# Kernel tuning notes

Measured on AMD Instinct MI355X. Metric: run time of the kernel, lower is better.

## Reference

```python
import jax, jax.numpy as jnp
import numpy as np

B, N, NFEAT = 64, 384, 16
E = 3
NHID, NOUT = 128, 128
ST_HID, ST_OUT = 64, 16


def _xavier(key, shape, fan_in, fan_out):
    a = jnp.sqrt(6.0 / (fan_in + fan_out))
    return jax.random.uniform(key, shape, jnp.float32, -a, a)


def setup_inputs() -> dict:
    key = jax.random.key(0)
    ks = jax.random.split(key, 10)
    x = jax.random.normal(ks[0], (B, N, NFEAT), jnp.float32)
    adj = jax.random.uniform(ks[1], (B, E, N, N), jnp.float32)
    emb_w = _xavier(ks[2], (NFEAT, NFEAT), NFEAT, NFEAT)            # Linear(nfeat,nfeat,bias=False)
    gc1_w = _xavier(ks[3], (E, NFEAT, NHID), NFEAT, NHID)           # (edge_dim,in,out)
    gc2_w = _xavier(ks[4], (E, NHID, NHID), NHID, NHID)             # single middle layer (num_layers-2=1)
    gc3_w = _xavier(ks[5], (E, NHID, NOUT), NHID, NOUT)
    st_w1 = _xavier(ks[6], (ST_HID, NOUT), NOUT, ST_HID)            # nn.Linear stores (out,in)
    st_b1 = jnp.zeros((ST_HID,), jnp.float32)
    st_w2 = jnp.full((2 * ST_OUT, ST_HID), 1e-10, jnp.float32)      # init.constant_(linear2.weight, 1e-10)
    st_b2 = jnp.zeros((2 * ST_OUT,), jnp.float32)
    rescale_w = jnp.zeros((1,), jnp.float32)                        # Rescale weight init zero
    return {"x": x, "adj": adj, "emb_w": emb_w, "gc1_w": gc1_w, "gc2_w": gc2_w,
            "gc3_w": gc3_w, "st_w1": st_w1, "st_b1": st_b1, "st_w2": st_w2,
            "st_b2": st_b2, "rescale_w": rescale_w}


def _rgcn_layer(h, adj, W, relu):
    # support: einsum('bid,edh->beih'), aggregate: einsum('beij,bejh->beih'), then sum over e
    support = jnp.einsum('bnd,edh->benh', h, W)
    out = jnp.einsum('bemn,benh->bemh', adj, support)
    if relu:
        out = jax.nn.relu(out)
    return out.sum(axis=1)  # aggregate='sum' over edge types


def reference(x, adj, emb_w, gc1_w, gc2_w, gc3_w, st_w1, st_b1, st_w2, st_b2, rescale_w):
    h = x @ emb_w.T                                   # emb Linear, no bias
    h = _rgcn_layer(h, adj, gc1_w, True)
    h = _rgcn_layer(h, adj, gc2_w, True)
    h = _rgcn_layer(h, adj, gc3_w, False)             # gc3: use_relu=False
    flat = h.reshape(-1, h.shape[-1])                 # (B*N, nout)
    z = jnp.tanh(flat @ st_w1.T + st_b1) @ st_w2.T + st_b2
    s, t = z[:, :ST_OUT], z[:, ST_OUT:]
    s = jnp.exp(rescale_w) * jnp.tanh(s)              # Rescale(tanh(s))
    return jnp.stack([s, t])                          # (2, B*N, ST_OUT)
```

## Files before the change

### kernel.cpp

```cpp
#include <hip/hip_runtime.h>
#include <math.h>

#define ROWS 24576
#define ADJ_BE (384*384)

typedef _Float16 h4v __attribute__((ext_vector_type(4)));
typedef _Float16 h8v __attribute__((ext_vector_type(8)));
typedef float f32x4 __attribute__((ext_vector_type(4)));

#define SPLIT_SCALE 2048.0f
#define INV_SPLIT_SCALE (1.0f / 2048.0f)

__global__ __launch_bounds__(256) void k_h0split(const float* __restrict__ x,
        const float* __restrict__ emb_w, _Float16* __restrict__ Hh, _Float16* __restrict__ Hl) {
    __shared__ float embL[256];
    int t = threadIdx.x;
    if (t < 64) *(float4*)&embL[4 * t] = *(const float4*)(emb_w + 4 * t);
    __syncthreads();
    int gid = blockIdx.x * 256 + t;
    int b = gid / 384, r = gid % 384;
    const float* xp = x + (size_t)gid * 16;
    float xr[16];
    *(float4*)&xr[0]  = *(const float4*)(xp);
    *(float4*)&xr[4]  = *(const float4*)(xp + 4);
    *(float4*)&xr[8]  = *(const float4*)(xp + 8);
    *(float4*)&xr[12] = *(const float4*)(xp + 12);
    size_t base = (size_t)b * 16 * 384 + r;
#pragma unroll
    for (int d = 0; d < 16; ++d) {
        float acc = 0.f;
#pragma unroll
        for (int k = 0; k < 16; ++k) acc = fmaf(xr[k], embL[d * 16 + k], acc);
        _Float16 h = (_Float16)acc;
        Hh[base + (size_t)d * 384] = h;
        Hl[base + (size_t)d * 384] = (_Float16)((acc - (float)h) * SPLIT_SCALE);
    }
}

__global__ __launch_bounds__(256) void k_adj16(const float* __restrict__ adj,
        const _Float16* __restrict__ Hh, const _Float16* __restrict__ Hl,
        float* __restrict__ T1) {
    int mt = blockIdx.x, e = blockIdx.y, b = blockIdx.z;
    const float* A = adj + (size_t)(b * 3 + e) * ADJ_BE + (size_t)mt * 64 * 384;
    const _Float16* BH = Hh + (size_t)b * 16 * 384;
    const _Float16* BL = Hl + (size_t)b * 16 * 384;

    __shared__ _Float16 Af[2][4][4][17][8];

    int t = threadIdx.x;
    int wave = t >> 6, lane = t & 63;
    int l16 = lane & 15, quad = lane >> 4;
    int r0s = t >> 3, q4s = t & 7;

    f32x4 acc0 = f32x4{0.f, 0.f, 0.f, 0.f};
    f32x4 acc1 = f32x4{0.f, 0.f, 0.f, 0.f};

    float4 ra[2];
    h8v rbh, rbl;
#pragma unroll
    for (int p = 0; p < 2; ++p)
        ra[p] = *(const float4*)(A + (size_t)(r0s + 32 * p) * 384 + 4 * q4s);
    rbh = *(const h8v*)(BH + (size_t)l16 * 384 + 8 * quad);
    rbl = *(const h8v*)(BL + (size_t)l16 * 384 + 8 * quad);

    for (int kc = 0; kc < 12; ++kc) {
#pragma unroll
        for (int p = 0; p < 2; ++p) {
            int r = r0s + 32 * p;
            float vv[4] = {ra[p].x, ra[p].y, ra[p].z, ra[p].w};
            h4v hh, ll;
#pragma unroll
            for (int c = 0; c < 4; ++c) {
                _Float16 h = (_Float16)vv[c];
                hh[c] = h;
                ll[c] = (_Float16)((vv[c] - (float)h) * SPLIT_SCALE);
            }
            *(h4v*)&Af[0][r >> 4][q4s >> 1][r & 15][(q4s & 1) * 4] = hh;
            *(h4v*)&Af[1][r >> 4][q4s >> 1][r & 15][(q4s & 1) * 4] = ll;
        }
        h8v b_h = rbh, b_l = rbl;
        __syncthreads();
        if (kc + 1 < 12) {
            int kn = (kc + 1) * 32;
#pragma unroll
            for (int p = 0; p < 2; ++p)
                ra[p] = *(const float4*)(A + (size_t)(r0s + 32 * p) * 384 + kn + 4 * q4s);
            rbh = *(const h8v*)(BH + (size_t)l16 * 384 + kn + 8 * quad);
            rbl = *(const h8v*)(BL + (size_t)l16 * 384 + kn + 8 * quad);
        }
        h8v a_h = *(const h8v*)&Af[0][wave][quad][l16][0];
        h8v a_l = *(const h8v*)&Af[1][wave][quad][l16][0];
        acc0 = __builtin_amdgcn_mfma_f32_16x16x32_f16(a_h, b_h, acc0, 0, 0, 0);
        acc1 = __builtin_amdgcn_mfma_f32_16x16x32_f16(a_h, b_l, acc1, 0, 0, 0);
        acc1 = __builtin_amdgcn_mfma_f32_16x16x32_f16(a_l, b_h, acc1, 0, 0, 0);
        __syncthreads();
    }
    float* Tp = T1 + ((size_t)(b * 3 + e) * 384 + (size_t)mt * 64 + wave * 16) * 16;
#pragma unroll
    for (int reg = 0; reg < 4; ++reg) {
        float v = fmaf(acc1[reg], INV_SPLIT_SCALE, acc0[reg]);
        Tp[(quad * 4 + reg) * 16 + l16] = v;
    }
}

__global__ __launch_bounds__(256) void k_l1s2(const float* __restrict__ T1,
        const float* __restrict__ W1, float* __restrict__ h1) {
    __shared__ float wL[3][16][128];
    __shared__ float tL[3][64][17];
    int t = threadIdx.x;
    int rt = blockIdx.x;
    int b = rt / 6, m0 = (rt % 6) * 64;
#pragma unroll
    for (int p = 0; p < 6; ++p) {
        int idx = t + p * 256;
        float4 v = *(const float4*)(W1 + (size_t)idx * 4);
        int e = idx / 512, rem = idx % 512;
        int d = rem >> 5, q = rem & 31;
        *(float4*)&wL[e][d][q * 4] = v;
    }
#pragma unroll
    for (int p = 0; p < 3; ++p) {
        int idx = t + p * 256;
        int e = idx >> 8, rem = idx & 255;
        int r = rem >> 2, q = rem & 3;
        float4 v = *(const float4*)(T1 + ((size_t)(b * 3 + e) * 384 + m0 + r) * 16 + q * 4);
        tL[e][r][q*4+0] = v.x; tL[e][r][q*4+1] = v.y; tL[e][r][q*4+2] = v.z; tL[e][r][q*4+3] = v.w;
    }
    __syncthreads();
    int tx = t & 31;
    int ty = t >> 5;
    float tot[8][4] = {};
#pragma unroll
    for (int e = 0; e < 3; ++e) {
        float acc[8][4] = {};
#pragma unroll
        for (int d = 0; d < 16; ++d) {
            float a[8], w[4];
#pragma unroll
            for (int i = 0; i < 8; ++i) a[i] = tL[e][ty + 8 * i][d];
#pragma unroll
            for (int j = 0; j < 4; ++j) w[j] = wL[e][d][tx + 32 * j];
#pragma unroll
            for (int i = 0; i < 8; ++i)
#pragma unroll
                for (int j = 0; j < 4; ++j)
                    acc[i][j] = fmaf(a[i], w[j], acc[i][j]);
        }
#pragma unroll
        for (int i = 0; i < 8; ++i)
#pragma unroll
            for (int j = 0; j < 4; ++j)
                tot[i][j] += fmaxf(acc[i][j], 0.f);
    }
    float* out = h1 + (size_t)rt * 64 * 128;
#pragma unroll
    for (int i = 0; i < 8; ++i)
#pragma unroll
        for (int j = 0; j < 4; ++j)
            out[(ty + 8 * i) * 128 + tx + 32 * j] = tot[i][j];
}

__global__ __launch_bounds__(256) void k_support(const float* __restrict__ hin,
        const float* __restrict__ W, _Float16* __restrict__ Sh, _Float16* __restrict__ Sl) {
    int rt = blockIdx.x, e = blockIdx.y;
    int b = rt / 6, n0 = (rt % 6) * 64;
    const float* Hp = hin + (size_t)rt * 64 * 128;
    const float* Wp = W + (size_t)e * 128 * 128;
    __shared__ float aT[32][68];
    __shared__ float bT[32][132];
    int t = threadIdx.x;
    int tx = t & 15;
    int ty = t >> 4;
    float acc[4][8] = {};
    for (int k0 = 0; k0 < 128; k0 += 32) {
        __syncthreads();
#pragma unroll
        for (int p = 0; p < 2; ++p) {
            int idx = t + p * 256;
            int r = idx >> 3, q = idx & 7;
            float4 v = *(const float4*)(Hp + (size_t)r * 128 + k0 + q * 4);
            aT[q*4+0][r] = v.x; aT[q*4+1][r] = v.y; aT[q*4+2][r] = v.z; aT[q*4+3][r] = v.w;
        }
#pragma unroll
        for (int p = 0; p < 4; ++p) {
            int idx = t + p * 256;
            int r = idx >> 5, q = idx & 31;
            *(float4*)&bT[r][q * 4] = *(const float4*)(Wp + (size_t)(k0 + r) * 128 + q * 4);
        }
        __syncthreads();
#pragma unroll
        for (int k = 0; k < 32; ++k) {
            float4 av = *(const float4*)&aT[k][4 * ty];
            float4 b0 = *(const float4*)&bT[k][4 * tx];
            float4 b1 = *(const float4*)&bT[k][64 + 4 * tx];
            float a[4] = {av.x, av.y, av.z, av.w};
            float bb[8] = {b0.x, b0.y, b0.z, b0.w, b1.x, b1.y, b1.z, b1.w};
#pragma unroll
            for (int i = 0; i < 4; ++i)
#pragma unroll
                for (int j = 0; j < 8; ++j)
                    acc[i][j] = fmaf(a[i], bb[j], acc[i][j]);
        }
    }
    size_t base = (size_t)(b * 3 + e) * 128 * 384;
#pragma unroll
    for (int j = 0; j < 8; ++j) {
        int n = (j < 4) ? (4 * tx + j) : (64 + 4 * tx + j - 4);
        h4v hh, ll;
#pragma unroll
        for (int i = 0; i < 4; ++i) {
            float v = acc[i][j];
            _Float16 h = (_Float16)v;
            hh[i] = h;
            ll[i] = (_Float16)((v - (float)h) * SPLIT_SCALE);
        }
        size_t off = base + (size_t)n * 384 + n0 + 4 * ty;
        *(h4v*)(Sh + off) = hh;
        *(h4v*)(Sl + off) = ll;
    }
}

template <int RELU>
__global__ __launch_bounds__(256, 2) void k_adj_fused(const float* __restrict__ adj,
        const _Float16* __restrict__ Sh, const _Float16* __restrict__ Sl,
        float* __restrict__ out) {
    int bid = blockIdx.x;
    int xcd = bid & 7, l = bid >> 3;
    int b = xcd * 8 + (l >> 3);
    int mt = l & 7;
    const float* A0 = adj + (size_t)(b * 3) * ADJ_BE + (size_t)mt * 48 * 384;
    const _Float16* Bh0 = Sh + (size_t)(b * 3) * 128 * 384;
    const _Float16* Bl0 = Sl + (size_t)(b * 3) * 128 * 384;
    float* O = out + ((size_t)b * 384 + mt * 48) * 128;

    __shared__ _Float16 Af[2][3][4][17][8];
    __shared__ _Float16 Bf[2][8][4][17][8];

    int t = threadIdx.x;
    int wave = t >> 6, lane = t & 63;
    int l16 = lane & 15, quad = lane >> 4;
    int r0s = t >> 3, q4s = t & 7;

    f32x4 acc0[3][2], acc1[3][2], tot[3][2];
#pragma unroll
    for (int i = 0; i < 3; ++i)
#pragma unroll
        for (int j = 0; j < 2; ++j) {
            acc0[i][j] = f32x4{0.f, 0.f, 0.f, 0.f};
            acc1[i][j] = f32x4{0.f, 0.f, 0.f, 0.f};
            tot[i][j]  = f32x4{0.f, 0.f, 0.f, 0.f};
        }

    float4 ra[2];
    h8v rb[4];

    const float* Ap = A0;
    const _Float16* Bhp = Bh0;
    const _Float16* Blp = Bl0;
    int kn = 0;

#pragma unroll
    for (int p = 0; p < 2; ++p)
        if (p == 0 || t < 128)
            ra[p] = *(const float4*)(Ap + (size_t)(r0s + 32 * p) * 384 + kn + 4 * q4s);
#pragma unroll
    for (int p = 0; p < 4; ++p) {
        int si = t + 256 * (p & 1);
        int n = si >> 2, q8 = si & 3;
        const _Float16* Bsrc = (p < 2) ? Bhp : Blp;
        rb[p] = *(const h8v*)(Bsrc + (size_t)n * 384 + kn + 8 * q8);
    }
    kn += 32;

    for (int c = 0; c < 36; ++c) {
#pragma unroll
        for (int p = 0; p < 2; ++p) {
            if (p == 1 && t >= 128) break;
            int r = r0s + 32 * p;
            float vv[4] = {ra[p].x, ra[p].y, ra[p].z, ra[p].w};
            h4v hh, ll;
#pragma unroll
            for (int cc = 0; cc < 4; ++cc) {
                _Float16 h = (_Float16)vv[cc];
                hh[cc] = h;
                ll[cc] = (_Float16)((vv[cc] - (float)h) * SPLIT_SCALE);
            }
            *(h4v*)&Af[0][r >> 4][q4s >> 1][r & 15][(q4s & 1) * 4] = hh;
            *(h4v*)&Af[1][r >> 4][q4s >> 1][r & 15][(q4s & 1) * 4] = ll;
        }
#pragma unroll
        for (int p = 0; p < 4; ++p) {
            int si = t + 256 * (p & 1);
            int n = si >> 2, q8 = si & 3;
            *(h8v*)&Bf[p >> 1][n >> 4][q8][n & 15][0] = rb[p];
        }
        __syncthreads();
        if (c + 1 < 36) {
            if (kn == 384) {
                kn = 0;
                Ap += (size_t)ADJ_BE;
                Bhp += (size_t)128 * 384;
                Blp += (size_t)128 * 384;
            }
#pragma unroll
            for (int p = 0; p < 2; ++p)
                if (p == 0 || t < 128)
                    ra[p] = *(const float4*)(Ap + (size_t)(r0s + 32 * p) * 384 + kn + 4 * q4s);
#pragma unroll
            for (int p = 0; p < 4; ++p) {
                int si = t + 256 * (p & 1);
                int n = si >> 2, q8 = si & 3;
                const _Float16* Bsrc = (p < 2) ? Bhp : Blp;
                rb[p] = *(const h8v*)(Bsrc + (size_t)n * 384 + kn + 8 * q8);
            }
            kn += 32;
        }
        h8v a_h[3], a_l[3];
#pragma unroll
        for (int i = 0; i < 3; ++i) {
            a_h[i] = *(const h8v*)&Af[0][i][quad][l16][0];
            a_l[i] = *(const h8v*)&Af[1][i][quad][l16][0];
        }
#pragma unroll
        for (int j = 0; j < 2; ++j) {
            h8v b_h = *(const h8v*)&Bf[0][2 * wave + j][quad][l16][0];
            h8v b_l = *(const h8v*)&Bf[1][2 * wave + j][quad][l16][0];
#pragma unroll
            for (int i = 0; i < 3; ++i) {
                acc0[i][j] = __builtin_amdgcn_mfma_f32_16x16x32_f16(a_h[i], b_h, acc0[i][j], 0, 0, 0);
                acc1[i][j] = __builtin_amdgcn_mfma_f32_16x16x32_f16(a_h[i], b_l, acc1[i][j], 0, 0, 0);
                acc1[i][j] = __builtin_amdgcn_mfma_f32_16x16x32_f16(a_l[i], b_h, acc1[i][j], 0, 0, 0);
            }
        }
        if (c % 12 == 11) {
#pragma unroll
            for (int i = 0; i < 3; ++i)
#pragma unroll
                for (int j = 0; j < 2; ++j) {
#pragma unroll
                    for (int reg = 0; reg < 4; ++reg) {
                        float v = fmaf(acc1[i][j][reg], INV_SPLIT_SCALE, acc0[i][j][reg]);
                        if (RELU) v = fmaxf(v, 0.f);
                        tot[i][j][reg] += v;
                    }
                    acc0[i][j] = f32x4{0.f, 0.f, 0.f, 0.f};
                    acc1[i][j] = f32x4{0.f, 0.f, 0.f, 0.f};
                }
        }
        __syncthreads();
    }
#pragma unroll
    for (int i = 0; i < 3; ++i) {
        int r0 = 16 * i + quad * 4;
#pragma unroll
        for (int j = 0; j < 2; ++j) {
            int gc = 32 * wave + 16 * j + l16;
#pragma unroll
            for (int reg = 0; reg < 4; ++reg)
                O[(size_t)(r0 + reg) * 128 + gc] = tot[i][j][reg];
        }
    }
}

__global__ __launch_bounds__(256) void k_head(const float* __restrict__ h3,
        const float* __restrict__ st_w1, const float* __restrict__ st_b1,
        const float* __restrict__ st_w2, const float* __restrict__ st_b2,
        const float* __restrict__ rescale_w, float* __restrict__ out) {
    __shared__ float hL[64][132];
    __shared__ float w1L[64][132];
    __shared__ float ytL[64][68];
    __shared__ float w2L[32][68];
    __shared__ float b1L[64], b2L[32];
    int t = threadIdx.x;
    int r0 = blockIdx.x * 64;
#pragma unroll
    for (int p = 0; p < 8; ++p) {
        int idx = t + p * 256;
        int r = idx >> 5, q = idx & 31;
        *(float4*)&hL[r][q * 4] = *(const float4*)(h3 + (size_t)(r0 + r) * 128 + q * 4);
    }
#pragma unroll
    for (int p = 0; p < 8; ++p) {
        int idx = t + p * 256;
        int r = idx >> 5, q = idx & 31;
        *(float4*)&w1L[r][q * 4] = *(const float4*)(st_w1 + (size_t)r * 128 + q * 4);
    }
#pragma unroll
    for (int p = 0; p < 2; ++p) {
        int idx = t + p * 256;
        int r = idx >> 4, q = idx & 15;
        *(float4*)&w2L[r][q * 4] = *(const float4*)(st_w2 + (size_t)r * 64 + q * 4);
    }
    if (t < 64) b1L[t] = st_b1[t];
    else if (t < 96) b2L[t - 64] = st_b2[t - 64];
    __syncthreads();
    int tx = t & 15, ty = t >> 4;
    float acc[4][4] = {};
    for (int d = 0; d < 128; ++d) {
        float a[4], w[4];
#pragma unroll
        for (int i = 0; i < 4; ++i) a[i] = hL[ty + 16 * i][d];
#pragma unroll
        for (int j = 0; j < 4; ++j) w[j] = w1L[tx + 16 * j][d];
#pragma unroll
        for (int i = 0; i < 4; ++i)
#pragma unroll
            for (int j = 0; j < 4; ++j)
                acc[i][j] = fmaf(a[i], w[j], acc[i][j]);
    }
#pragma unroll
    for (int i = 0; i < 4; ++i)
#pragma unroll
        for (int j = 0; j < 4; ++j)
            ytL[ty + 16 * i][tx + 16 * j] = tanhf(acc[i][j] + b1L[tx + 16 * j]);
    __syncthreads();
    int tx8 = t & 7, ty32 = t >> 3;
    float acc2[2][4] = {};
    for (int d = 0; d < 64; ++d) {
        float a[2], w[4];
#pragma unroll
        for (int i = 0; i < 2; ++i) a[i] = ytL[ty32 + 32 * i][d];
#pragma unroll
        for (int j = 0; j < 4; ++j) w[j] = w2L[tx8 + 8 * j][d];
#pragma unroll
        for (int i = 0; i < 2; ++i)
#pragma unroll
            for (int j = 0; j < 4; ++j)
                acc2[i][j] = fmaf(a[i], w[j], acc2[i][j]);
    }
    float er = expf(rescale_w[0]);
#pragma unroll
    for (int i = 0; i < 2; ++i) {
        int r = r0 + ty32 + 32 * i;
#pragma unroll
        for (int j = 0; j < 4; ++j) {
            int c = tx8 + 8 * j;
            float z = acc2[i][j] + b2L[c];
            if (c < 16) out[(size_t)r * 16 + c] = er * tanhf(z);
            else        out[(size_t)(ROWS + r) * 16 + (c - 16)] = z;
        }
    }
}

extern "C" void kernel_launch(void* const* d_in, const int* in_sizes, int n_in,
                              void* d_out, int out_size, void* d_ws, size_t ws_size,
                              hipStream_t stream) {
    const float* x     = (const float*)d_in[0];
    const float* adj   = (const float*)d_in[1];
    const float* emb_w = (const float*)d_in[2];
    const float* gc1   = (const float*)d_in[3];
    const float* gc2   = (const float*)d_in[4];
    const float* gc3   = (const float*)d_in[5];
    const float* st_w1 = (const float*)d_in[6];
    const float* st_b1 = (const float*)d_in[7];
    const float* st_w2 = (const float*)d_in[8];
    const float* st_b2 = (const float*)d_in[9];
    const float* resc  = (const float*)d_in[10];
    float* out = (float*)d_out;
    float* ws  = (float*)d_ws;

    float* T1 = ws;
    float* hA = T1 + 1179648;
    float* hB = hA + 3145728;
    _Float16* Sh = (_Float16*)(hB + 3145728);
    _Float16* Sl = Sh + 9437184;
    _Float16* Hh = (_Float16*)hB;
    _Float16* Hl = Hh + 393216;

    k_h0split<<<96, 256, 0, stream>>>(x, emb_w, Hh, Hl);
    k_adj16<<<dim3(6, 3, 64), 256, 0, stream>>>(adj, Hh, Hl, T1);
    k_l1s2<<<384, 256, 0, stream>>>(T1, gc1, hA);
    k_support<<<dim3(384, 3), 256, 0, stream>>>(hA, gc2, Sh, Sl);
    k_adj_fused<1><<<512, 256, 0, stream>>>(adj, Sh, Sl, hB);
    k_support<<<dim3(384, 3), 256, 0, stream>>>(hB, gc3, Sh, Sl);
    k_adj_fused<0><<<512, 256, 0, stream>>>(adj, Sh, Sl, hA);
    k_head<<<384, 256, 0, stream>>>(hA, st_w1, st_b1, st_w2, st_b2, resc, out);
}
```

Before: 374.8 us.

## Double-buffer LDS tiles in adjacency GEMM to drop one barrier per chunk

Turns the shared-memory A/B tiles into ping-pong buffers. The next chunk is staged into the alternate buffer after the MFMAs, and global loads are prefetched two chunks ahead. This removes one of the two __syncthreads per iteration and overlaps LDS staging with compute. In exchange it doubles LDS usage, roughly 39KB per block, which could limit occupancy at 2 blocks per CU. It also keeps prefetched registers live longer.

```diff
diff --git a/kernel.cpp b/kernel.cpp
--- a/kernel.cpp
+++ b/kernel.cpp
@@ -233,8 +233,8 @@
     const _Float16* Bl0 = Sl + (size_t)(b * 3) * 128 * 384;
     float* O = out + ((size_t)b * 384 + mt * 48) * 128;
 
-    __shared__ _Float16 Af[2][3][4][17][8];
-    __shared__ _Float16 Bf[2][8][4][17][8];
+    __shared__ _Float16 Af[2][2][3][4][17][8];
+    __shared__ _Float16 Bf[2][2][8][4][17][8];
 
     int t = threadIdx.x;
     int wave = t >> 6, lane = t & 63;
@@ -254,77 +254,67 @@
     float4 ra[2];
     h8v rb[4];
 
-    const float* Ap = A0;
-    const _Float16* Bhp = Bh0;
-    const _Float16* Blp = Bl0;
-    int kn = 0;
-
-#pragma unroll
-    for (int p = 0; p < 2; ++p)
-        if (p == 0 || t < 128)
-            ra[p] = *(const float4*)(Ap + (size_t)(r0s + 32 * p) * 384 + kn + 4 * q4s);
-#pragma unroll
-    for (int p = 0; p < 4; ++p) {
-        int si = t + 256 * (p & 1);
-        int n = si >> 2, q8 = si & 3;
-        const _Float16* Bsrc = (p < 2) ? Bhp : Blp;
-        rb[p] = *(const h8v*)(Bsrc + (size_t)n * 384 + kn + 8 * q8);
-    }
-    kn += 32;
-
+#define LOAD_CHUNK(cc)                                                              \
+    {                                                                               \
+        int e_ = (cc) / 12, kk_ = ((cc) % 12) * 32;                                 \
+        const float* Ap_ = A0 + (size_t)e_ * ADJ_BE;                                \
+        const _Float16* Bhp_ = Bh0 + (size_t)e_ * (128 * 384);                      \
+        const _Float16* Blp_ = Bl0 + (size_t)e_ * (128 * 384);                      \
+        _Pragma("unroll")                                                           \
+        for (int p = 0; p < 2; ++p)                                                 \
+            if (p == 0 || t < 128)                                                  \
+                ra[p] = *(const float4*)(Ap_ + (size_t)(r0s + 32 * p) * 384 + kk_ + 4 * q4s); \
+        _Pragma("unroll")                                                           \
+        for (int p = 0; p < 4; ++p) {                                               \
+            int si_ = t + 256 * (p & 1);                                            \
+            int n_ = si_ >> 2, q8_ = si_ & 3;                                       \
+            const _Float16* Bsrc_ = (p < 2) ? Bhp_ : Blp_;                          \
+            rb[p] = *(const h8v*)(Bsrc_ + (size_t)n_ * 384 + kk_ + 8 * q8_);        \
+        }                                                                           \
+    }
+
+#define STAGE_CHUNK(d)                                                              \
+    {                                                                               \
+        _Pragma("unroll")                                                           \
+        for (int p = 0; p < 2; ++p) {                                               \
+            if (p == 1 && t >= 128) break;                                          \
+            int r_ = r0s + 32 * p;                                                  \
+            float vv_[4] = {ra[p].x, ra[p].y, ra[p].z, ra[p].w};                    \
+            h4v hh_, ll_;                                                           \
+            _Pragma("unroll")                                                       \
+            for (int cc_ = 0; cc_ < 4; ++cc_) {                                     \
+                _Float16 h_ = (_Float16)vv_[cc_];                                   \
+                hh_[cc_] = h_;                                                      \
+                ll_[cc_] = (_Float16)((vv_[cc_] - (float)h_) * SPLIT_SCALE);        \
+            }                                                                       \
+            *(h4v*)&Af[d][0][r_ >> 4][q4s >> 1][r_ & 15][(q4s & 1) * 4] = hh_;      \
+            *(h4v*)&Af[d][1][r_ >> 4][q4s >> 1][r_ & 15][(q4s & 1) * 4] = ll_;      \
+        }                                                                           \
+        _Pragma("unroll")                                                           \
+        for (int p = 0; p < 4; ++p) {                                               \
+            int si_ = t + 256 * (p & 1);                                            \
+            int n_ = si_ >> 2, q8_ = si_ & 3;                                       \
+            *(h8v*)&Bf[d][p >> 1][n_ >> 4][q8_][n_ & 15][0] = rb[p];                \
+        }                                                                           \
+    }
+
+    LOAD_CHUNK(0);
+    STAGE_CHUNK(0);
+    LOAD_CHUNK(1);
+    __syncthreads();
+
+    int cur = 0;
     for (int c = 0; c < 36; ++c) {
-#pragma unroll
-        for (int p = 0; p < 2; ++p) {
-            if (p == 1 && t >= 128) break;
-            int r = r0s + 32 * p;
-            float vv[4] = {ra[p].x, ra[p].y, ra[p].z, ra[p].w};
-            h4v hh, ll;
-#pragma unroll
-            for (int cc = 0; cc < 4; ++cc) {
-                _Float16 h = (_Float16)vv[cc];
-                hh[cc] = h;
-                ll[cc] = (_Float16)((vv[cc] - (float)h) * SPLIT_SCALE);
-            }
-            *(h4v*)&Af[0][r >> 4][q4s >> 1][r & 15][(q4s & 1) * 4] = hh;
-            *(h4v*)&Af[1][r >> 4][q4s >> 1][r & 15][(q4s & 1) * 4] = ll;
-        }
-#pragma unroll
-        for (int p = 0; p < 4; ++p) {
-            int si = t + 256 * (p & 1);
-            int n = si >> 2, q8 = si & 3;
-            *(h8v*)&Bf[p >> 1][n >> 4][q8][n & 15][0] = rb[p];
-        }
-        __syncthreads();
-        if (c + 1 < 36) {
-            if (kn == 384) {
-                kn = 0;
-                Ap += (size_t)ADJ_BE;
-                Bhp += (size_t)128 * 384;
-                Blp += (size_t)128 * 384;
-            }
-#pragma unroll
-            for (int p = 0; p < 2; ++p)
-                if (p == 0 || t < 128)
-                    ra[p] = *(const float4*)(Ap + (size_t)(r0s + 32 * p) * 384 + kn + 4 * q4s);
-#pragma unroll
-            for (int p = 0; p < 4; ++p) {
-                int si = t + 256 * (p & 1);
-                int n = si >> 2, q8 = si & 3;
-                const _Float16* Bsrc = (p < 2) ? Bhp : Blp;
-                rb[p] = *(const h8v*)(Bsrc + (size_t)n * 384 + kn + 8 * q8);
-            }
-            kn += 32;
-        }
         h8v a_h[3], a_l[3];
 #pragma unroll
         for (int i = 0; i < 3; ++i) {
-            a_h[i] = *(const h8v*)&Af[0][i][quad][l16][0];
-            a_l[i] = *(const h8v*)&Af[1][i][quad][l16][0];
+            a_h[i] = *(const h8v*)&Af[cur][0][i][quad][l16][0];
+            a_l[i] = *(const h8v*)&Af[cur][1][i][quad][l16][0];
         }
 #pragma unroll
         for (int j = 0; j < 2; ++j) {
-            h8v b_h = *(const h8v*)&Bf[0][2 * wave + j][quad][l16][0];
-            h8v b_l = *(const h8v*)&Bf[1][2 * wave + j][quad][l16][0];
+            h8v b_h = *(const h8v*)&Bf[cur][0][2 * wave + j][quad][l16][0];
+            h8v b_l = *(const h8v*)&Bf[cur][1][2 * wave + j][quad][l16][0];
 #pragma unroll
             for (int i = 0; i < 3; ++i) {
                 acc0[i][j] = __builtin_amdgcn_mfma_f32_16x16x32_f16(a_h[i], b_h, acc0[i][j], 0, 0, 0);
@@ -332,6 +322,8 @@
                 acc1[i][j] = __builtin_amdgcn_mfma_f32_16x16x32_f16(a_l[i], b_h, acc1[i][j], 0, 0, 0);
             }
         }
+        if (c + 1 < 36) STAGE_CHUNK(cur ^ 1);
+        if (c + 2 < 36) LOAD_CHUNK(c + 2);
         if (c % 12 == 11) {
 #pragma unroll
             for (int i = 0; i < 3; ++i)
@@ -348,7 +340,10 @@
                 }
         }
         __syncthreads();
-    }
+        cur ^= 1;
+    }
+#undef LOAD_CHUNK
+#undef STAGE_CHUNK
 #pragma unroll
     for (int i = 0; i < 3; ++i) {
         int r0 = 16 * i + quad * 4;
```

Result: slower. 383.6 us (+2.3%).
